# Performance work log

Measured on AMD Instinct MI355X. Metric: run time of the kernel, lower is better.

Reference implementation:

```python
import jax, jax.numpy as jnp
import numpy as np

B, N_KP, DIM, STEP = 262144, 11, 2, 4


def setup_inputs() -> dict:
    key = jax.random.key(0)
    k1, k2, k3 = jax.random.split(key, 3)
    index = jnp.arange(N_KP, dtype=jnp.int32) * STEP  # keypoint frame indices [0,4,...,40]
    value = jax.random.normal(k1, (B, N_KP, DIM), dtype=jnp.float32)
    init_speed = jax.random.normal(k2, (B, 1, DIM), dtype=jnp.float32)
    init_acc = jax.random.normal(k3, (B, 1, DIM), dtype=jnp.float32)
    return {"index": index, "value": value, "init_speed": init_speed, "init_acc": init_acc}


def _interp(x, value, init_speed, init_acc):
    # x: concrete numpy int array of keypoint indices (static).
    # Closed form of the piecewise recurrence acc+=da; v+=acc; y+=v:
    #   acc_k = a0 + k*da
    #   v_k   = v0 + k*a0 + da*k(k+1)/2
    #   y_k   = y0 + k*v0 + a0*k(k+1)/2 + da*k(k+1)(k+2)/6
    # and torch's denominator n(n+1)/4 + n(n+1)(2n+1)/12 == n(n+1)(n+2)/6.
    v0, a0 = init_speed, init_acc
    outs = []
    for i in range(len(x) - 1):
        n = int(x[i + 1] - x[i])
        y0 = value[..., i:i + 1, :]
        y1 = value[..., i + 1:i + 2, :]
        dy = y1 - y0
        if n <= 1:
            outs.append(y1)
            new_v = y1 - y0
            a0 = new_v - v0
            v0 = new_v
            continue
        da = (dy - n * v0 - (n * (n + 1) / 2) * a0) / (n * (n + 1) * (n + 2) / 6)
        k = jnp.arange(1, n + 1, dtype=value.dtype)[:, None]  # (n, 1)
        # broadcast (n,1) against (..., 1, dim) -> (..., n, dim)
        pos = y0 + k * v0 + (k * (k + 1) / 2) * a0 + (k * (k + 1) * (k + 2) / 6) * da
        outs.append(pos)
        v0 = v0 + n * a0 + (n * (n + 1) / 2) * da
        a0 = a0 + n * da
    return jnp.concatenate(outs, axis=-2)  # (..., m, dim)


def reference(index, value, init_speed, init_acc):
    x = np.asarray(jax.device_get(index)).astype(np.int64)  # static keypoint indices
    return _interp(x, value, init_speed, init_acc)
```

## Files before the change

kernel.cpp:

```cpp
#include <hip/hip_runtime.h>


typedef float f4 __attribute__((ext_vector_type(4)));

template <int NSEG>
__global__ __launch_bounds__(256) void interp_fast(
    const int* __restrict__ index,
    const float2* __restrict__ value,
    const float2* __restrict__ vinit,
    const float2* __restrict__ ainit,
    float2* __restrict__ out,
    int B)
{
    constexpr int NKP  = NSEG + 1;
    constexpr int ROWS = 4 * NSEG;
    constexpr int PAD2 = ROWS + 2;
    constexpr int RF4  = ROWS / 2;
    constexpr int PF4  = PAD2 / 2;
    constexpr int WB   = 16;
    constexpr int WF2  = WB * NKP;

    __shared__ float2 lds2[64 * PAD2];
    __shared__ float2 svi[64];
    __shared__ float2 sai[64];

    int tid = threadIdx.x;
    int w   = tid >> 6;
    int l   = tid & 63;
    int first_b = blockIdx.x * 64;

    int xi[NKP];
#pragma unroll
    for (int i = 0; i < NKP; ++i) xi[i] = index[i];

    {
        const float2* gv = value + (long)first_b * NKP;
#pragma unroll
        for (int t = 0; t < (WF2 + 63) / 64; ++t) {
            int fo = t * 64 + l;
            if (fo < WF2) {
                int f  = w * WF2 + fo;
                int bb = f / NKP;
                int j  = f - bb * NKP;
                lds2[bb * PAD2 + j] = gv[f];
            }
        }
        int wb = w * WB;
        if (l < WB) svi[wb + l] = vinit[first_b + wb + l];
        else if (l < 2 * WB) sai[wb + l - WB] = ainit[first_b + wb + l - WB];
    }

    bool fast = true;
#pragma unroll
    for (int i = 0; i < NSEG; ++i) fast = fast && (xi[i + 1] - xi[i] == 4);

    int bl = tid >> 2;
    int r  = tid & 3;
    float2* __restrict__ row = lds2 + bl * PAD2;

    float2 y[NKP];
#pragma unroll
    for (int i = 0; i < NKP; ++i) y[i] = row[i];
    float2 v0 = svi[bl];
    float2 a0 = sai[bl];

    if (fast) {
#pragma unroll
        for (int i = 0; i < NSEG; ++i) {
            float2 y0 = y[i];
            float2 y1 = y[i + 1];
            float dyx = y1.x - y0.x;
            float dyy = y1.y - y0.y;
            float dax = (dyx - 4.0f * v0.x - 10.0f * a0.x) * 0.05f;
            float day = (dyy - 4.0f * v0.y - 10.0f * a0.y) * 0.05f;

            float fk = (float)(r + 1);
            float t2 = fk * (fk + 1.0f) * 0.5f;
            float t3 = t2 * (fk + 2.0f) * (1.0f / 3.0f);
            float2 p;
            p.x = y0.x + fk * v0.x + t2 * a0.x + t3 * dax;
            p.y = y0.y + fk * v0.y + t2 * a0.y + t3 * day;
            row[4 * i + r] = p;

            v0.x += 4.0f * a0.x + 10.0f * dax;
            v0.y += 4.0f * a0.y + 10.0f * day;
            a0.x += 4.0f * dax;
            a0.y += 4.0f * day;
        }
    } else {
        int off = 0;
#pragma unroll
        for (int i = 0; i < NSEG; ++i) {
            float2 y0 = y[i];
            float2 y1 = y[i + 1];
            int n = xi[i + 1] - xi[i];
            float dyx = y1.x - y0.x;
            float dyy = y1.y - y0.y;
            if (n <= 1) {
                if (r == 0) row[off] = y1;
                off += 1;
                a0.x = dyx - v0.x;
                a0.y = dyy - v0.y;
                v0.x = dyx;
                v0.y = dyy;
            } else {
                float fn = (float)n;
                float c1 = fn * (fn + 1.0f) * 0.5f;
                float c2 = fn * (fn + 1.0f) * (fn + 2.0f) / 6.0f;
                float rc2 = __builtin_amdgcn_rcpf(c2);
                float dax = (dyx - fn * v0.x - c1 * a0.x) * rc2;
                float day = (dyy - fn * v0.y - c1 * a0.y) * rc2;
                for (int k = r + 1; k <= n; k += 4) {
                    float fk = (float)k;
                    float t2 = fk * (fk + 1.0f) * 0.5f;
                    float t3 = fk * (fk + 1.0f) * (fk + 2.0f) * (1.0f / 6.0f);
                    float2 p;
                    p.x = y0.x + fk * v0.x + t2 * a0.x + t3 * dax;
                    p.y = y0.y + fk * v0.y + t2 * a0.y + t3 * day;
                    if (off + k - 1 < ROWS) row[off + k - 1] = p;
                }
                off += n;
                v0.x += fn * a0.x + c1 * dax;
                v0.y += fn * a0.y + c1 * day;
                a0.x += fn * dax;
                a0.y += fn * day;
            }
        }
    }

    {
        const f4* __restrict__ l4 = (const f4*)lds2;
        f4* __restrict__ o4 = (f4*)out + (long)first_b * RF4;
        int c0 = w * WB * RF4;
#pragma unroll
        for (int m = 0; m < WB * RF4 / 64; ++m) {
            int c  = c0 + m * 64 + l;
            int bb = c / RF4;
            int j  = c - bb * RF4;
            o4[c] = l4[bb * PF4 + j];
        }
    }
}

__global__ __launch_bounds__(256) void interp_gen(
    const int* __restrict__ index,
    const float2* __restrict__ value,
    const float2* __restrict__ vinit,
    const float2* __restrict__ ainit,
    float2* __restrict__ out,
    int B, int nkp, int rows, int PT)
{
    long t = (long)blockIdx.x * 256 + threadIdx.x;
    long total = (long)B * PT;
    if (t >= total) return;
    int b = (int)(t / PT);
    int j = (int)(t - (long)b * PT);
    int g_lo = j * 8;
    int g_hi = g_lo + 8;
    if (g_hi > rows) g_hi = rows;

    const float2* __restrict__ vrow = value + (long)b * nkp;
    float2* __restrict__ orow = out + (long)b * rows;
    float2 v0 = vinit[b];
    float2 a0 = ainit[b];
    float2 y0 = vrow[0];
    int x0 = index[0];
    int off = 0;
    for (int i = 0; i < nkp - 1; ++i) {
        float2 y1 = vrow[i + 1];
        int x1 = index[i + 1];
        int n = x1 - x0; x0 = x1;
        float dyx = y1.x - y0.x, dyy = y1.y - y0.y;
        if (n <= 1) {
            if (off >= g_lo && off < g_hi) orow[off] = y1;
            off += 1;
            a0.x = dyx - v0.x; a0.y = dyy - v0.y;
            v0.x = dyx; v0.y = dyy;
        } else {
            float fn = (float)n;
            float c1 = fn * (fn + 1.0f) * 0.5f;
            float c2 = fn * (fn + 1.0f) * (fn + 2.0f) / 6.0f;
            float dax = (dyx - fn * v0.x - c1 * a0.x) / c2;
            float day = (dyy - fn * v0.y - c1 * a0.y) / c2;
            for (int k = 1; k <= n; ++k) {
                int g = off + k - 1;
                if (g >= g_lo && g < g_hi) {
                    float fk = (float)k;
                    float t2 = fk * (fk + 1.0f) * 0.5f;
                    float t3 = fk * (fk + 1.0f) * (fk + 2.0f) * (1.0f / 6.0f);
                    float2 p;
                    p.x = y0.x + fk * v0.x + t2 * a0.x + t3 * dax;
                    p.y = y0.y + fk * v0.y + t2 * a0.y + t3 * day;
                    orow[g] = p;
                }
            }
            off += n;
            v0.x += fn * a0.x + c1 * dax;
            v0.y += fn * a0.y + c1 * day;
            a0.x += fn * dax;
            a0.y += fn * day;
        }
        y0 = y1;
    }
}

extern "C" void kernel_launch(void* const* d_in, const int* in_sizes, int n_in,
                              void* d_out, int out_size, void* d_ws, size_t ws_size,
                              hipStream_t stream) {
    const int*    index = (const int*)d_in[0];
    const float2* value = (const float2*)d_in[1];
    const float2* vinit = (const float2*)d_in[2];
    const float2* ainit = (const float2*)d_in[3];
    float2*       out   = (float2*)d_out;

    int nkp  = in_sizes[0];
    int B    = in_sizes[1] / (nkp * 2);
    int rows = out_size / (B * 2);

    if (nkp == 11 && rows == 40 && (B % 64) == 0) {
        dim3 grid(B / 64);
        interp_fast<10><<<grid, 256, 0, stream>>>(index, value, vinit, ainit, out, B);
    } else {
        int PT = (rows + 7) / 8;
        long total = (long)B * PT;
        dim3 grid((unsigned)((total + 255) / 256));
        interp_gen<<<grid, 256, 0, stream>>>(index, value, vinit, ainit, out, B, nkp, rows, PT);
    }
}
```

Baseline: 25.09 us.

## Replace LDS output staging with quad swizzle transposes and direct nontemporal stores

The fast path no longer stages results in shared memory before a coalesced copy-out. Each quad of lanes computes two segments at a time and uses ds_swizzle quad permutes to gather four contiguous float2 outputs per lane, then writes them straight to global memory with 16-byte nontemporal stores. This removes the LDS write/read round trip and the padded output buffer, leaving shared memory only for the input values. The cost is extra select and swizzle instructions and a store pattern where each row is written by four lanes, which may coalesce less well than the old block-wide copy.

```diff
diff --git a/kernel.cpp b/kernel.cpp
--- a/kernel.cpp
+++ b/kernel.cpp
@@ -2,6 +2,11 @@
 
 
 typedef float f4 __attribute__((ext_vector_type(4)));
+
+template <int PAT>
+__device__ __forceinline__ float swz(float x) {
+    return __int_as_float(__builtin_amdgcn_ds_swizzle(__float_as_int(x), PAT));
+}
 
 template <int NSEG>
 __global__ __launch_bounds__(256) void interp_fast(
@@ -14,13 +19,13 @@
 {
     constexpr int NKP  = NSEG + 1;
     constexpr int ROWS = 4 * NSEG;
-    constexpr int PAD2 = ROWS + 2;
     constexpr int RF4  = ROWS / 2;
-    constexpr int PF4  = PAD2 / 2;
     constexpr int WB   = 16;
     constexpr int WF2  = WB * NKP;
-
-    __shared__ float2 lds2[64 * PAD2];
+    constexpr int QP1  = 0x808D;
+    constexpr int QP2  = 0x80D8;
+
+    __shared__ float2 sv[64 * NKP];
     __shared__ float2 svi[64];
     __shared__ float2 sai[64];
 
@@ -39,10 +44,8 @@
         for (int t = 0; t < (WF2 + 63) / 64; ++t) {
             int fo = t * 64 + l;
             if (fo < WF2) {
-                int f  = w * WF2 + fo;
-                int bb = f / NKP;
-                int j  = f - bb * NKP;
-                lds2[bb * PAD2 + j] = gv[f];
+                int f = w * WF2 + fo;
+                sv[f] = gv[f];
             }
         }
         int wb = w * WB;
@@ -56,7 +59,7 @@
 
     int bl = tid >> 2;
     int r  = tid & 3;
-    float2* __restrict__ row = lds2 + bl * PAD2;
+    const float2* __restrict__ row = sv + bl * NKP;
 
     float2 y[NKP];
 #pragma unroll
@@ -65,29 +68,62 @@
     float2 a0 = sai[bl];
 
     if (fast) {
-#pragma unroll
-        for (int i = 0; i < NSEG; ++i) {
-            float2 y0 = y[i];
-            float2 y1 = y[i + 1];
+        float fk = (float)(r + 1);
+        float t2 = fk * (fk + 1.0f) * 0.5f;
+        float t3 = t2 * (fk + 2.0f) * (1.0f / 3.0f);
+
+        f4* __restrict__ o4 = (f4*)out + (long)first_b * RF4 + bl * RF4 + r;
+
+#pragma unroll
+        for (int j = 0; j < NSEG / 2; ++j) {
+            float2 y0 = y[2 * j];
+            float2 y1 = y[2 * j + 1];
             float dyx = y1.x - y0.x;
             float dyy = y1.y - y0.y;
             float dax = (dyx - 4.0f * v0.x - 10.0f * a0.x) * 0.05f;
             float day = (dyy - 4.0f * v0.y - 10.0f * a0.y) * 0.05f;
-
-            float fk = (float)(r + 1);
-            float t2 = fk * (fk + 1.0f) * 0.5f;
-            float t3 = t2 * (fk + 2.0f) * (1.0f / 3.0f);
             float2 p;
             p.x = y0.x + fk * v0.x + t2 * a0.x + t3 * dax;
             p.y = y0.y + fk * v0.y + t2 * a0.y + t3 * day;
-            row[4 * i + r] = p;
-
             v0.x += 4.0f * a0.x + 10.0f * dax;
             v0.y += 4.0f * a0.y + 10.0f * day;
             a0.x += 4.0f * dax;
             a0.y += 4.0f * day;
+
+            float2 z0 = y1;
+            float2 z1 = y[2 * j + 2];
+            float dzx = z1.x - z0.x;
+            float dzy = z1.y - z0.y;
+            float dbx = (dzx - 4.0f * v0.x - 10.0f * a0.x) * 0.05f;
+            float dby = (dzy - 4.0f * v0.y - 10.0f * a0.y) * 0.05f;
+            float2 pp;
+            pp.x = z0.x + fk * v0.x + t2 * a0.x + t3 * dbx;
+            pp.y = z0.y + fk * v0.y + t2 * a0.y + t3 * dby;
+            v0.x += 4.0f * a0.x + 10.0f * dbx;
+            v0.y += 4.0f * a0.y + 10.0f * dby;
+            a0.x += 4.0f * dbx;
+            a0.y += 4.0f * dby;
+
+            bool odd = (r & 1);
+            float o1x = odd ? p.x : pp.x;
+            float o1y = odd ? p.y : pp.y;
+            float t1x = swz<QP1>(o1x);
+            float t1y = swz<QP1>(o1y);
+            float o2x = (r == 2) ? p.x : pp.x;
+            float o2y = (r == 2) ? p.y : pp.y;
+            float t2x = swz<QP2>(o2x);
+            float t2y = swz<QP2>(o2y);
+
+            f4 o;
+            o.x = (r == 0) ? p.x : (r == 1) ? t2x : t1x;
+            o.y = (r == 0) ? p.y : (r == 1) ? t2y : t1y;
+            o.z = (r < 2) ? t1x : (r == 2) ? t2x : pp.x;
+            o.w = (r < 2) ? t1y : (r == 2) ? t2y : pp.y;
+
+            __builtin_nontemporal_store(o, o4 + 4 * j);
         }
     } else {
+        float2* __restrict__ orow = out + ((long)first_b + bl) * ROWS;
         int off = 0;
 #pragma unroll
         for (int i = 0; i < NSEG; ++i) {
@@ -97,7 +133,7 @@
             float dyx = y1.x - y0.x;
             float dyy = y1.y - y0.y;
             if (n <= 1) {
-                if (r == 0) row[off] = y1;
+                if (r == 0 && off < ROWS) orow[off] = y1;
                 off += 1;
                 a0.x = dyx - v0.x;
                 a0.y = dyy - v0.y;
@@ -111,13 +147,16 @@
                 float dax = (dyx - fn * v0.x - c1 * a0.x) * rc2;
                 float day = (dyy - fn * v0.y - c1 * a0.y) * rc2;
                 for (int k = r + 1; k <= n; k += 4) {
-                    float fk = (float)k;
-                    float t2 = fk * (fk + 1.0f) * 0.5f;
-                    float t3 = fk * (fk + 1.0f) * (fk + 2.0f) * (1.0f / 6.0f);
-                    float2 p;
-                    p.x = y0.x + fk * v0.x + t2 * a0.x + t3 * dax;
-                    p.y = y0.y + fk * v0.y + t2 * a0.y + t3 * day;
-                    if (off + k - 1 < ROWS) row[off + k - 1] = p;
+                    int g = off + k - 1;
+                    if (g < ROWS) {
+                        float gk = (float)k;
+                        float g2 = gk * (gk + 1.0f) * 0.5f;
+                        float g3 = gk * (gk + 1.0f) * (gk + 2.0f) * (1.0f / 6.0f);
+                        float2 q;
+                        q.x = y0.x + gk * v0.x + g2 * a0.x + g3 * dax;
+                        q.y = y0.y + gk * v0.y + g2 * a0.y + g3 * day;
+                        orow[g] = q;
+                    }
                 }
                 off += n;
                 v0.x += fn * a0.x + c1 * dax;
@@ -125,19 +164,6 @@
                 a0.x += fn * dax;
                 a0.y += fn * day;
             }
-        }
-    }
-
-    {
-        const f4* __restrict__ l4 = (const f4*)lds2;
-        f4* __restrict__ o4 = (f4*)out + (long)first_b * RF4;
-        int c0 = w * WB * RF4;
-#pragma unroll
-        for (int m = 0; m < WB * RF4 / 64; ++m) {
-            int c  = c0 + m * 64 + l;
-            int bb = c / RF4;
-            int j  = c - bb * RF4;
-            o4[c] = l4[bb * PF4 + j];
         }
     }
 }
@@ -185,12 +211,12 @@
             for (int k = 1; k <= n; ++k) {
                 int g = off + k - 1;
                 if (g >= g_lo && g < g_hi) {
-                    float fk = (float)k;
-                    float t2 = fk * (fk + 1.0f) * 0.5f;
-                    float t3 = fk * (fk + 1.0f) * (fk + 2.0f) * (1.0f / 6.0f);
+                    float fkk = (float)k;
+                    float t2 = fkk * (fkk + 1.0f) * 0.5f;
+                    float t3 = fkk * (fkk + 1.0f) * (fkk + 2.0f) * (1.0f / 6.0f);
                     float2 p;
-                    p.x = y0.x + fk * v0.x + t2 * a0.x + t3 * dax;
-                    p.y = y0.y + fk * v0.y + t2 * a0.y + t3 * day;
+                    p.x = y0.x + fkk * v0.x + t2 * a0.x + t3 * dax;
+                    p.y = y0.y + fkk * v0.y + t2 * a0.y + t3 * day;
                     orow[g] = p;
                 }
             }
```

Measured after the change: 28.46 us. +13.4%, slower.
